# Kernel tuning notes

Measured on AMD Instinct MI355X. Metric: run time of the kernel, lower is better.

Reference implementation:

```python
import jax, jax.numpy as jnp
import numpy as np

B, CIN, COUT, H, W = 8, 128, 128, 64, 64
KH = KW = 3
STRIDE = PAD = 1
DIL = 1
K = KH * KW
EPS = 1e-4


def setup_inputs() -> dict:
    key = jax.random.key(0)
    k1, k2, k3 = jax.random.split(key, 3)
    Ho = (H + 2 * PAD - DIL * (KH - 1) - 1) // STRIDE + 1
    Wo = (W + 2 * PAD - DIL * (KW - 1) - 1) // STRIDE + 1
    x = jax.random.normal(k1, (B, CIN, H, W), dtype=jnp.float32)
    offset = jax.random.normal(k2, (B, 2 * K, Ho, Wo), dtype=jnp.float32)
    weight = jax.random.normal(k3, (COUT, CIN, KH, KW), dtype=jnp.float32) * 0.05
    return {"x": x, "offset": offset, "weight": weight}


def _bilinear_gather(x, py, px):
    # x: [B, C, H, W]; py/px: [B, K, Ho, Wo] float sampling positions
    Bn, C, Hn, Wn = x.shape
    x_flat = x.reshape(Bn, C, Hn * Wn)
    y0 = jnp.floor(py)
    x0 = jnp.floor(px)
    ly = py - y0  # fractional parts
    lx = px - x0
    out = 0.0
    corners = [(0.0, 0.0, (1 - ly) * (1 - lx)), (0.0, 1.0, (1 - ly) * lx),
               (1.0, 0.0, ly * (1 - lx)), (1.0, 1.0, ly * lx)]
    for dy, dx, wgt in corners:
        yy = y0 + dy
        xx = x0 + dx
        valid = (yy >= 0) & (yy < Hn) & (xx >= 0) & (xx < Wn)
        yi = jnp.clip(yy, 0, Hn - 1).astype(jnp.int32)
        xi = jnp.clip(xx, 0, Wn - 1).astype(jnp.int32)
        idx = (yi * Wn + xi).reshape(Bn, -1)  # [B, K*Ho*Wo]
        g = jax.vmap(lambda xf, ib: jnp.take(xf, ib, axis=1))(x_flat, idx)  # [B, C, N]
        out = out + g * (wgt * valid.astype(x.dtype)).reshape(Bn, 1, -1)
    return out  # [B, C, K*Ho*Wo]


def reference(x, offset, weight) -> jnp.ndarray:
    Bn = x.shape[0]
    Ho, Wo = offset.shape[2], offset.shape[3]
    # --- weight normalization (per output channel, per kernel tap) ---
    norm_fac = (KH * KW) ** 0.5
    length = jnp.sqrt(jnp.sum(jnp.square(weight) + EPS, axis=1, keepdims=True))  # [O,1,kh,kw]
    wn = weight / length / norm_fac  # [O, Cin, kh, kw]
    # --- sampling positions ---
    off = offset.reshape(Bn, K, 2, Ho, Wo)
    off_y, off_x = off[:, :, 0], off[:, :, 1]
    ky, kx = jnp.meshgrid(jnp.arange(KH), jnp.arange(KW), indexing="ij")
    ky = (ky.reshape(K) * DIL).astype(jnp.float32)
    kx = (kx.reshape(K) * DIL).astype(jnp.float32)
    base_y = (jnp.arange(Ho) * STRIDE - PAD).astype(jnp.float32)
    base_x = (jnp.arange(Wo) * STRIDE - PAD).astype(jnp.float32)
    py = base_y[None, None, :, None] + ky[None, :, None, None] + off_y  # [B,K,Ho,Wo]
    px = base_x[None, None, None, :] + kx[None, :, None, None] + off_x
    # --- deformable im2col + GEMM ---
    cols = _bilinear_gather(x, py, px).reshape(Bn, CIN, K, Ho, Wo)
    out = jnp.einsum("bckhw,ock->bohw", cols, wn.reshape(COUT, CIN, K))
    return out
```

## Files before the change

kernel.cpp:

```cpp
#include <hip/hip_runtime.h>
#include <hip/hip_bf16.h>
#include <hip/hip_fp16.h>
#include <math.h>


typedef __attribute__((ext_vector_type(8))) short short8;
typedef __attribute__((ext_vector_type(4))) float floatx4;
typedef __attribute__((ext_vector_type(2))) float floatx2;

static __device__ __forceinline__ unsigned int f2bf(float f) {
    unsigned int u = __float_as_uint(f);
    u += 0x7fffu + ((u >> 16) & 1u);
    return u >> 16;
}
static __device__ __forceinline__ unsigned int packbf2(float lo, float hi) {
    __hip_bfloat162 h = __float22bfloat162_rn(make_float2(lo, hi));
    unsigned int u;
    __builtin_memcpy(&u, &h, 4);
    return u;
}
static __device__ __forceinline__ floatx2 bf2f2(unsigned int w) {
    floatx2 r;
    r.x = __uint_as_float(w << 16);
    r.y = __uint_as_float(w & 0xffff0000u);
    return r;
}

__global__ void prep_k(const float* __restrict__ x, const float* __restrict__ w,
                       unsigned int* __restrict__ xt32, unsigned short* __restrict__ wb) {
    __shared__ float lds[128 * 65];
    const int tid = threadIdx.x;

    if (blockIdx.x < 512) {
        const int b = blockIdx.x & 7, h = (blockIdx.x >> 3) & 63;
        const float* xp = x + (b * 128 * 64 + h) * 64;
        #pragma unroll 4
        for (int i = 0; i < 32; i++) {
            const int c = i * 4 + (tid >> 6);
            const int ww = tid & 63;
            lds[c * 65 + ww] = xp[c * 4096 + ww];
        }
        __syncthreads();
        unsigned int* xo = xt32 + (b * 64 + h) * 4096;
        #pragma unroll 4
        for (int i = 0; i < 16; i++) {
            const int flat2 = i * 256 + tid;
            const int ww = flat2 >> 6, cp = flat2 & 63;
            xo[flat2] = packbf2(lds[(2 * cp) * 65 + ww], lds[(2 * cp + 1) * 65 + ww]);
        }
    } else {
        const int o = (blockIdx.x - 512) * 4 + (tid >> 6);
        const int lane = tid & 63;
        const float* wo = w + o * 1152;
        float v[18];
        #pragma unroll
        for (int i = 0; i < 18; i++) v[i] = wo[lane * 18 + i];
        float s[9];
        #pragma unroll
        for (int k = 0; k < 9; k++) s[k] = v[k] * v[k] + v[9 + k] * v[9 + k];
        #pragma unroll
        for (int d = 32; d >= 1; d >>= 1) {
            #pragma unroll
            for (int k = 0; k < 9; k++) s[k] += __shfl_xor(s[k], d, 64);
        }
        const int c0 = 2 * lane, c1 = c0 + 1;
        #pragma unroll
        for (int k = 0; k < 9; k++) {
            const float inv = 1.0f / (3.0f * sqrtf(s[k] + 0.0128f));
            wb[((k * 16 + (c0 >> 3)) * 128 + o) * 8 + (c0 & 7)] = (unsigned short)f2bf(v[k] * inv);
            wb[((k * 16 + (c1 >> 3)) * 128 + o) * 8 + (c1 & 7)] = (unsigned short)f2bf(v[9 + k] * inv);
        }
    }
}

static __device__ __forceinline__ unsigned int bl1(const float4 w,
                                                   unsigned int r0, unsigned int r1,
                                                   unsigned int r2, unsigned int r3) {
    floatx2 a = bf2f2(r0) * w.x;
    a += bf2f2(r1) * w.y;
    a += bf2f2(r2) * w.z;
    a += bf2f2(r3) * w.w;
    return packbf2(a.x, a.y);
}

static __device__ __forceinline__ uint4 combine4(const float4 wvv,
                                                 const uint4 r0, const uint4 r1,
                                                 const uint4 r2, const uint4 r3) {
    uint4 pk;
    pk.x = bl1(wvv, r0.x, r1.x, r2.x, r3.x);
    pk.y = bl1(wvv, r0.y, r1.y, r2.y, r3.y);
    pk.z = bl1(wvv, r0.z, r1.z, r2.z, r3.z);
    pk.w = bl1(wvv, r0.w, r1.w, r2.w, r3.w);
    return pk;
}

static __device__ __forceinline__ void rec_expand(const uint4 rec, float4& wvv, int4& iv) {
    const float2 w01 = __half22float2(*reinterpret_cast<const __half2*>(&rec.x));
    const float2 w23 = __half22float2(*reinterpret_cast<const __half2*>(&rec.y));
    wvv = make_float4(w01.x, w01.y, w23.x, w23.y);
    iv = make_int4((int)(rec.z & 0xffffu) << 7, (int)(rec.z >> 16) << 7,
                   (int)(rec.w & 0xffffu) << 7, (int)(rec.w >> 16) << 7);
}

__global__ __launch_bounds__(512, 4) void dconv_k(
    const unsigned short* __restrict__ xt, const float* __restrict__ off,
    const unsigned short* __restrict__ wb, float* __restrict__ out)
{
    __shared__ alignas(16) uint4 tapG[576];
    __shared__ alignas(16) unsigned short colsS[2][16 * 520];

    const int idx = blockIdx.x;
    const int b = idx & 7;
    const int ho = (idx >> 3) & 63;
    const int tid = threadIdx.x;

    for (int t = tid; t < 576; t += 512) {
        const int k = t >> 6, p = t & 63;
        const int oidx = ((b * 18 + 2 * k) * 64 + ho) * 64 + p;
        const float offy = off[oidx];
        const float offx = off[oidx + 4096];
        const float py = (float)(ho - 1 + (k / 3)) + offy;
        const float px = (float)(p - 1 + (k % 3)) + offx;
        const float y0f = floorf(py), x0f = floorf(px);
        const float ly = py - y0f, lx = px - x0f;
        const int y0 = (int)y0f, x0 = (int)x0f;
        const int y1 = y0 + 1, x1 = x0 + 1;
        const float fy0 = (y0 >= 0 && y0 < 64) ? (1.0f - ly) : 0.0f;
        const float fy1 = (y1 >= 0 && y1 < 64) ? ly : 0.0f;
        const float fx0 = (x0 >= 0 && x0 < 64) ? (1.0f - lx) : 0.0f;
        const float fx1 = (x1 >= 0 && x1 < 64) ? lx : 0.0f;
        const int yc0 = min(max(y0, 0), 63), yc1 = min(max(y1, 0), 63);
        const int xc0 = min(max(x0, 0), 63), xc1 = min(max(x1, 0), 63);
        const __half2 a01 = __float22half2_rn(make_float2(fy0 * fx0, fy0 * fx1));
        const __half2 a23 = __float22half2_rn(make_float2(fy1 * fx0, fy1 * fx1));
        uint4 pk;
        __builtin_memcpy(&pk.x, &a01, 4);
        __builtin_memcpy(&pk.y, &a23, 4);
        pk.z = (unsigned int)(yc0 * 64 + xc0) | ((unsigned int)(yc0 * 64 + xc1) << 16);
        pk.w = (unsigned int)(yc1 * 64 + xc0) | ((unsigned int)(yc1 * 64 + xc1) << 16);
        tapG[t] = pk;
    }
    __syncthreads();

    const int lane = tid & 63, wv = tid >> 6;
    const int quad = lane >> 4, l16 = lane & 15;
    const int g = tid & 15, p0 = tid >> 4;
    const unsigned short* xb = xt + b * (64 * 64 * 128);
    const int ph = wv & 1,  cq = wv >> 1;
    const int pbase = ph * 32;
    const int obase = cq * 32;

    floatx4 acc[4];
    #pragma unroll
    for (int t = 0; t < 4; t++) acc[t] = (floatx4)0.0f;

    #pragma unroll
    for (int i = 0; i < 2; i++) {
        const int p = p0 + i * 32;
        float4 wvv; int4 iv;
        rec_expand(tapG[p], wvv, iv);
        const uint4 r0 = *(const uint4*)(xb + iv.x + g * 8);
        const uint4 r1 = *(const uint4*)(xb + iv.y + g * 8);
        const uint4 r2 = *(const uint4*)(xb + iv.z + g * 8);
        const uint4 r3 = *(const uint4*)(xb + iv.w + g * 8);
        *(uint4*)&colsS[0][g * 520 + p * 8] = combine4(wvv, r0, r1, r2, r3);
    }
    __syncthreads();

    for (int k = 0; k < 9; k++) {
        const int cur = k & 1;

        const unsigned short* wk = wb + k * 16384;
        short8 a[8];
        #pragma unroll
        for (int q = 0; q < 4; q++) {
            const int cgrp = q * 4 + quad;
            #pragma unroll
            for (int n = 0; n < 2; n++)
                a[q * 2 + n] = *(const short8*)(wk + (cgrp * 128 + obase + n * 16 + l16) * 8);
        }

        uint4 r[2][4];
        float4 wvv[2];
        if (k < 8) {
            #pragma unroll
            for (int i = 0; i < 2; i++) {
                const int p = p0 + i * 32;
                int4 iv;
                rec_expand(tapG[(k + 1) * 64 + p], wvv[i], iv);
                r[i][0] = *(const uint4*)(xb + iv.x + g * 8);
                r[i][1] = *(const uint4*)(xb + iv.y + g * 8);
                r[i][2] = *(const uint4*)(xb + iv.z + g * 8);
                r[i][3] = *(const uint4*)(xb + iv.w + g * 8);
            }
        }

        #pragma unroll
        for (int q = 0; q < 4; q++) {
            const int cgrp = q * 4 + quad;
            const short8 bf0 = *(const short8*)&colsS[cur][cgrp * 520 + (pbase + l16) * 8];
            const short8 bf1 = *(const short8*)&colsS[cur][cgrp * 520 + (pbase + 16 + l16) * 8];
            acc[0] = __builtin_amdgcn_mfma_f32_16x16x32_bf16(a[q * 2 + 0], bf0, acc[0], 0, 0, 0);
            acc[1] = __builtin_amdgcn_mfma_f32_16x16x32_bf16(a[q * 2 + 1], bf0, acc[1], 0, 0, 0);
            acc[2] = __builtin_amdgcn_mfma_f32_16x16x32_bf16(a[q * 2 + 0], bf1, acc[2], 0, 0, 0);
            acc[3] = __builtin_amdgcn_mfma_f32_16x16x32_bf16(a[q * 2 + 1], bf1, acc[3], 0, 0, 0);
        }

        if (k < 8) {
            #pragma unroll
            for (int i = 0; i < 2; i++) {
                const int p = p0 + i * 32;
                *(uint4*)&colsS[cur ^ 1][g * 520 + p * 8] =
                    combine4(wvv[i], r[i][0], r[i][1], r[i][2], r[i][3]);
            }
            __syncthreads();
        }
    }

    float* ob = out + b * 128 * 4096 + ho * 64;
    #pragma unroll
    for (int t = 0; t < 2; t++) {
        const int pix = pbase + t * 16 + l16;
        #pragma unroll
        for (int n = 0; n < 2; n++) {
            #pragma unroll
            for (int r2 = 0; r2 < 4; r2++) {
                __builtin_nontemporal_store(acc[t * 2 + n][r2],
                    &ob[(obase + n * 16 + quad * 4 + r2) * 4096 + pix]);
            }
        }
    }
}

extern "C" void kernel_launch(void* const* d_in, const int* in_sizes, int n_in,
                              void* d_out, int out_size, void* d_ws, size_t ws_size,
                              hipStream_t stream) {
    const float* x   = (const float*)d_in[0];
    const float* off = (const float*)d_in[1];
    const float* w   = (const float*)d_in[2];
    float* out = (float*)d_out;

    unsigned short* xt = (unsigned short*)d_ws;
    unsigned short* wbuf = xt + 8 * 64 * 64 * 128;

    hipLaunchKernelGGL(prep_k,  dim3(544), dim3(256), 0, stream,
                       x, w, (unsigned int*)xt, wbuf);
    hipLaunchKernelGGL(dconv_k, dim3(512), dim3(512), 0, stream, xt, off, wbuf, out);
}
```

Baseline: 101.4 us.

## Deepen gather prefetch to two taps ahead and use LDS-only barrier

Moves the gather pipeline one tap further ahead: the combine/store of tap k+1 into the alternate LDS buffer happens at the start of iteration k, and the global loads for tap k+2 are issued before the MFMA loop. This gives the bilinear gather loads a full iteration of MFMA work to hide latency. It also replaces __syncthreads with a barrier that waits only on LDS counters, so outstanding global loads are not drained at each barrier. It costs extra registers for the in-flight gather data, which may pressure occupancy under the 512x4 launch bounds.

```diff
diff --git a/kernel.cpp b/kernel.cpp
--- a/kernel.cpp
+++ b/kernel.cpp
@@ -100,6 +100,12 @@
     wvv = make_float4(w01.x, w01.y, w23.x, w23.y);
     iv = make_int4((int)(rec.z & 0xffffu) << 7, (int)(rec.z >> 16) << 7,
                    (int)(rec.w & 0xffffu) << 7, (int)(rec.w >> 16) << 7);
+}
+
+static __device__ __forceinline__ void lds_barrier() {
+    asm volatile("s_waitcnt lgkmcnt(0)" ::: "memory");
+    __builtin_amdgcn_s_barrier();
+    asm volatile("" ::: "memory");
 }
 
 __global__ __launch_bounds__(512, 4) void dconv_k(
@@ -154,18 +160,31 @@
     #pragma unroll
     for (int t = 0; t < 4; t++) acc[t] = (floatx4)0.0f;
 
+    uint4 r[2][4];
+    float4 wvv[2];
+
     #pragma unroll
     for (int i = 0; i < 2; i++) {
         const int p = p0 + i * 32;
-        float4 wvv; int4 iv;
-        rec_expand(tapG[p], wvv, iv);
-        const uint4 r0 = *(const uint4*)(xb + iv.x + g * 8);
-        const uint4 r1 = *(const uint4*)(xb + iv.y + g * 8);
-        const uint4 r2 = *(const uint4*)(xb + iv.z + g * 8);
-        const uint4 r3 = *(const uint4*)(xb + iv.w + g * 8);
-        *(uint4*)&colsS[0][g * 520 + p * 8] = combine4(wvv, r0, r1, r2, r3);
-    }
-    __syncthreads();
+        float4 w0; int4 iv;
+        rec_expand(tapG[p], w0, iv);
+        const uint4 c0 = *(const uint4*)(xb + iv.x + g * 8);
+        const uint4 c1 = *(const uint4*)(xb + iv.y + g * 8);
+        const uint4 c2 = *(const uint4*)(xb + iv.z + g * 8);
+        const uint4 c3 = *(const uint4*)(xb + iv.w + g * 8);
+        *(uint4*)&colsS[0][g * 520 + p * 8] = combine4(w0, c0, c1, c2, c3);
+    }
+    #pragma unroll
+    for (int i = 0; i < 2; i++) {
+        const int p = p0 + i * 32;
+        int4 iv;
+        rec_expand(tapG[64 + p], wvv[i], iv);
+        r[i][0] = *(const uint4*)(xb + iv.x + g * 8);
+        r[i][1] = *(const uint4*)(xb + iv.y + g * 8);
+        r[i][2] = *(const uint4*)(xb + iv.z + g * 8);
+        r[i][3] = *(const uint4*)(xb + iv.w + g * 8);
+    }
+    lds_barrier();
 
     for (int k = 0; k < 9; k++) {
         const int cur = k & 1;
@@ -180,14 +199,21 @@
                 a[q * 2 + n] = *(const short8*)(wk + (cgrp * 128 + obase + n * 16 + l16) * 8);
         }
 
-        uint4 r[2][4];
-        float4 wvv[2];
         if (k < 8) {
+            #pragma unroll
+            for (int i = 0; i < 2; i++) {
+                const int p = p0 + i * 32;
+                *(uint4*)&colsS[cur ^ 1][g * 520 + p * 8] =
+                    combine4(wvv[i], r[i][0], r[i][1], r[i][2], r[i][3]);
+            }
+        }
+
+        if (k < 7) {
             #pragma unroll
             for (int i = 0; i < 2; i++) {
                 const int p = p0 + i * 32;
                 int4 iv;
-                rec_expand(tapG[(k + 1) * 64 + p], wvv[i], iv);
+                rec_expand(tapG[(k + 2) * 64 + p], wvv[i], iv);
                 r[i][0] = *(const uint4*)(xb + iv.x + g * 8);
                 r[i][1] = *(const uint4*)(xb + iv.y + g * 8);
                 r[i][2] = *(const uint4*)(xb + iv.z + g * 8);
@@ -206,15 +232,7 @@
             acc[3] = __builtin_amdgcn_mfma_f32_16x16x32_bf16(a[q * 2 + 1], bf1, acc[3], 0, 0, 0);
         }
 
-        if (k < 8) {
-            #pragma unroll
-            for (int i = 0; i < 2; i++) {
-                const int p = p0 + i * 32;
-                *(uint4*)&colsS[cur ^ 1][g * 520 + p * 8] =
-                    combine4(wvv[i], r[i][0], r[i][1], r[i][2], r[i][3]);
-            }
-            __syncthreads();
-        }
+        if (k < 8) lds_barrier();
     }
 
     float* ob = out + b * 128 * 4096 + ho * 64;
```

After: 99.03 us. -2.3%, faster.
